# Performance work log

Measured on AMD Instinct MI355X. Metric: run time of the kernel, lower is better.

## Reference

```python
import jax, jax.numpy as jnp
from jax import lax
import numpy as np

B, T, H, W = 32, 16, 64, 64
LAT, HID, NL = 256, 256, 10
CH = 32  # c_hid
DN = ('NCHW', 'OIHW', 'NCHW')


def setup_inputs() -> dict:
    key = jax.random.key(0)
    keys = iter(jax.random.split(key, 64))
    def rn(shape, scale=0.05):
        return jax.random.normal(next(keys), shape, jnp.float32) * scale
    inp = {}
    inp['x'] = jax.random.normal(next(keys), (B, T, H, W), jnp.float32)
    inp['t'] = jax.random.normal(next(keys), (B, T, H, W), jnp.float32)
    # encoder convs (torch Conv2d weight layout: (out,in,kh,kw))
    inp['ec1_w'] = rn((CH, 1, 3, 3));        inp['ec1_b'] = rn((CH,))
    inp['ec2_w'] = rn((CH, CH, 3, 3));       inp['ec2_b'] = rn((CH,))
    inp['ec3_w'] = rn((2*CH, CH, 3, 3));     inp['ec3_b'] = rn((2*CH,))
    inp['ec4_w'] = rn((2*CH, 2*CH, 3, 3));   inp['ec4_b'] = rn((2*CH,))
    inp['ec5_w'] = rn((2*CH, 2*CH, 3, 3));   inp['ec5_b'] = rn((2*CH,))
    inp['el_w'] = rn((LAT, 2*CH*8*8));       inp['el_b'] = rn((LAT,))
    # decoder (ConvTranspose2d weight layout: (in,out,kh,kw))
    inp['dl_w'] = rn((2*CH*8*8, LAT));       inp['dl_b'] = rn((2*CH*8*8,))
    inp['dt1_w'] = rn((2*CH, 2*CH, 3, 3));   inp['dt1_b'] = rn((2*CH,))
    inp['dc1_w'] = rn((2*CH, 2*CH, 3, 3));   inp['dc1_b'] = rn((2*CH,))
    inp['dt2_w'] = rn((2*CH, CH, 3, 3));     inp['dt2_b'] = rn((CH,))
    inp['dc2_w'] = rn((CH, CH, 3, 3));       inp['dc2_b'] = rn((CH,))
    inp['dt3_w'] = rn((CH, 1, 3, 3));        inp['dt3_b'] = rn((1,))
    # 10 stacked LSTMCells (LAT == HID so layer 0 weight shape matches the rest)
    inp['Wih'] = rn((NL, 4*HID, HID))
    inp['Whh'] = rn((NL, 4*HID, HID))
    inp['bih'] = rn((NL, 4*HID))
    inp['bhh'] = rn((NL, 4*HID))
    inp['lw'] = rn((LAT, HID));  inp['lb'] = rn((LAT,))
    return inp


def gelu(v):
    return jax.nn.gelu(v, approximate=False)


def conv(x, w, b, stride):
    y = lax.conv_general_dilated(x, w, (stride, stride), [(1, 1), (1, 1)], dimension_numbers=DN)
    return y + b[None, :, None, None]


def tconv(x, w, b):
    # torch ConvTranspose2d(k=3, stride=2, padding=1, output_padding=1):
    # flip kernel, swap in/out channels, lhs_dilation=2, pad (lo=1, hi=2)
    wf = jnp.transpose(w[:, :, ::-1, ::-1], (1, 0, 2, 3))
    y = lax.conv_general_dilated(x, wf, (1, 1), [(1, 2), (1, 2)], lhs_dilation=(2, 2), dimension_numbers=DN)
    return y + b[None, :, None, None]


def reference(x, t, ec1_w, ec1_b, ec2_w, ec2_b, ec3_w, ec3_b, ec4_w, ec4_b, ec5_w, ec5_b,
              el_w, el_b, dl_w, dl_b, dt1_w, dt1_b, dc1_w, dc1_b, dt2_w, dt2_b,
              dc2_w, dc2_b, dt3_w, dt3_b, Wih, Whh, bih, bhh, lw, lb):

    def encode(imgs):                              # (N,1,64,64) -> (N,LAT)
        h = gelu(conv(imgs, ec1_w, ec1_b, 2))      # 32x32
        h = gelu(conv(h, ec2_w, ec2_b, 1))
        h = gelu(conv(h, ec3_w, ec3_b, 2))         # 16x16
        h = gelu(conv(h, ec4_w, ec4_b, 1))
        h = gelu(conv(h, ec5_w, ec5_b, 2))         # 8x8
        return h.reshape(h.shape[0], -1) @ el_w.T + el_b

    def decode(z):                                 # (N,LAT) -> (N,1,64,64)
        h = gelu(z @ dl_w.T + dl_b).reshape(z.shape[0], 2*CH, 8, 8)
        h = gelu(tconv(h, dt1_w, dt1_b))           # 16x16
        h = gelu(conv(h, dc1_w, dc1_b, 1))
        h = gelu(tconv(h, dt2_w, dt2_b))           # 32x32
        h = gelu(conv(h, dc2_w, dc2_b, 1))
        return jnp.tanh(tconv(h, dt3_w, dt3_b))    # 64x64

    def cell_stack(h, c, xin):                     # h,c: (NL,B,HID)
        hs, cs = [], []
        prev = xin
        for l in range(NL):
            z = prev @ Wih[l].T + bih[l] + h[l] @ Whh[l].T + bhh[l]
            i, f, g, o = jnp.split(z, 4, axis=-1)
            cl = jax.nn.sigmoid(f) * c[l] + jax.nn.sigmoid(i) * jnp.tanh(g)
            hl = jax.nn.sigmoid(o) * jnp.tanh(cl)
            hs.append(hl); cs.append(cl); prev = hl
        out = prev @ lw.T + lb                     # skip=False
        return jnp.stack(hs), jnp.stack(cs), out

    f_x_t = jnp.concatenate((x, t), axis=1)        # (B,2T,H,W)
    z_x_t = encode(f_x_t.reshape(-1, 1, H, W)).reshape(B, 2 * T, LAT)
    z_x = z_x_t[:, :T]

    h0 = jnp.zeros((NL, B, HID), x.dtype)
    c0 = jnp.zeros((NL, B, HID), x.dtype)

    def step1(carry, xin):
        h, c = carry
        h, c, out = cell_stack(h, c, xin)
        return (h, c), out

    (hT, cT), outs1 = lax.scan(step1, (h0, c0), jnp.swapaxes(z_x, 0, 1))

    def step2(carry, _):
        h, c, xin = carry
        h, c, out = cell_stack(h, c, xin)
        return (h, c, out), out

    _, outs2 = lax.scan(step2, (hT, cT, outs1[-1]), None, length=T)

    outputs = jnp.swapaxes(jnp.concatenate((outs1, outs2), axis=0), 0, 1)  # (B,2T,LAT)
    y_t = outputs[:, T - 1:-1]                    # (B,T,LAT)

    f_t_ = decode(y_t.reshape(B * T, LAT))        # (B*T,1,H,W)
    loss_pred = jnp.mean((f_t_ - f_x_t[:, T:].reshape(-1, 1, H, W)) ** 2)

    f_x_ = decode(z_x.reshape(B * T, LAT))        # rec_loss=True branch
    loss_rec = jnp.mean((f_x_ - f_x_t[:, :T].reshape(-1, 1, H, W)) ** 2)

    return loss_pred, loss_rec, f_t_.reshape(B, T, H, W)
```

## Files before the change

kernel.cpp:

```cpp
#include <hip/hip_runtime.h>
#include <math.h>

#define DEV __device__ __forceinline__

typedef __attribute__((ext_vector_type(8))) short bf8_t;
typedef __attribute__((ext_vector_type(4))) float f4_t;
typedef unsigned short us;

DEV float sigm_f(float v) { return 1.0f / (1.0f + __expf(-v)); }
DEV float tanh_f(float v) { return fmaf(-2.0f, 1.0f / (1.0f + __expf(2.0f * v)), 1.0f); }
DEV float gelu_f(float v) {
  float u = 0.79788456080f * fmaf(0.044715f * v * v, v, v);
  return 0.5f * v * (1.0f + tanh_f(u));
}
DEV unsigned short f2bf(float f) {
  unsigned u = __float_as_uint(f);
  u = (u + 0x7FFFu + ((u >> 16) & 1u)) >> 16;
  return (unsigned short)u;
}
DEV void astore(unsigned* p, unsigned v) {
  __hip_atomic_store(p, v, __ATOMIC_RELAXED, __HIP_MEMORY_SCOPE_AGENT);
}

DEV void prep_norm(int li, const float* w, us* wb, int CIN) {
// ... 19 lines not shown
    const float* __restrict__ ec2, const float* __restrict__ ec3,
    const float* __restrict__ ec4, const float* __restrict__ ec5,
    const float* __restrict__ dt1, const float* __restrict__ dc1,
    const float* __restrict__ dt2, const float* __restrict__ dc2,
    us* __restrict__ o_ec2, us* __restrict__ o_ec3,
    us* __restrict__ o_ec4, us* __restrict__ o_ec5,
    us* __restrict__ o_dt1, us* __restrict__ o_dc1,
    us* __restrict__ o_dt2, us* __restrict__ o_dc2)
{
  int idx = blockIdx.x * 256 + threadIdx.x;
  if (idx < 9216)        prep_norm(idx,          ec2, o_ec2, 32);
  else if (idx < 27648)  prep_norm(idx - 9216,   ec3, o_ec3, 32);
  else if (idx < 64512)  prep_norm(idx - 27648,  ec4, o_ec4, 64);
  else if (idx < 101376) prep_norm(idx - 64512,  ec5, o_ec5, 64);
  else if (idx < 138240) prep_par (idx - 101376, dt1, o_dt1, 64, 64);
  else if (idx < 175104) prep_norm(idx - 138240, dc1, o_dc1, 64);
  else if (idx < 193536) prep_par (idx - 175104, dt2, o_dt2, 32, 64);
  else if (idx < 202752) prep_norm(idx - 193536, dc2, o_dc2, 32);
}

__global__ __launch_bounds__(256) void prep_misc_k(
    const float* __restrict__ Wih, const float* __restrict__ lw,
    const float* __restrict__ lb,  const float* __restrict__ bih,
    us* __restrict__ wih0b, us* __restrict__ lwTb,
    us* __restrict__ lwbp,  float* __restrict__ beff)
{
  int idx = blockIdx.x * 256 + threadIdx.x;
  if (idx < 262144) {
    wih0b[idx] = f2bf(Wih[idx]);
  } else if (idx < 327680) {
    int i = idx - 262144;
    int n = i & 255, kcol = i >> 8;
    lwTb[i] = f2bf(lw[(size_t)n * 256 + kcol]);
  } else if (idx < 393216) {
    int i = idx - 327680;
    lwbp[i] = f2bf(lw[i]);
  } else if (idx < 394240) {
    int j = idx - 393216;
    float s = bih[j];
    const float* row = Wih + (size_t)j * 256;
    for (int n = 0; n < 256; ++n) s = fmaf(row[n], lb[n], s);
    beff[j] = s;
  }
}

__global__ __launch_bounds__(256) void prep_big_k(
    const float* __restrict__ el_w, const float* __restrict__ dl_w,
    const float* __restrict__ Wih,  const float* __restrict__ Whh,
    us* __restrict__ elWb, us* __restrict__ dlWb,
    us* __restrict__ wihb, us* __restrict__ whhb)
{
  int idx = blockIdx.x * 256 + threadIdx.x;
  if (idx < 1048576) {
    int i = idx;
    int kn = i & 4095, n = i >> 12;
    elWb[i] = f2bf(el_w[(size_t)n * 4096 + ((kn & 63) * 64 + (kn >> 6))]);
  } else if (idx < 2097152) {
    int i = idx - 1048576;
    int k = i & 255, nout = i >> 8;
    dlWb[i] = f2bf(dl_w[(size_t)((nout & 63) * 64 + (nout >> 6)) * 256 + k]);
  } else if (idx < 4718592) {
    int i = idx - 2097152;
    int e = i & 7, lane = (i >> 3) & 63, ks = (i >> 9) & 7;
    int nt = (i >> 12) & 63, l = i >> 18;
    wihb[i] = f2bf(Wih[((size_t)l * 1024 + nt * 16 + (lane & 15)) * 256
                       + ks * 32 + (lane >> 4) * 8 + e]);
  } else {
    int i = idx - 4718592;
    int e = i & 7, lane = (i >> 3) & 63, ks = (i >> 9) & 7;
    int nt = (i >> 12) & 63, l = i >> 18;
    whhb[i] = f2bf(Whh[((size_t)l * 1024 + nt * 16 + (lane & 15)) * 256
                       + ks * 32 + (lane >> 4) * 8 + e]);
  }
}

__global__ __launch_bounds__(256) void prep_wl1_k(
    const us* __restrict__ src, us* __restrict__ wb)
{
  int idx = blockIdx.x * 256 + threadIdx.x;
  int e = idx & 7, lane = (idx >> 3) & 63, ks = (idx >> 9) & 7, nt = idx >> 12;
  wb[idx] = src[(size_t)(nt * 16 + (lane & 15)) * 256 + ks * 32 + (lane >> 4) * 8 + e];
}

__global__ __launch_bounds__(256) void ec1_k(
    const float* __restrict__ x, const float* __restrict__ t,
    const float* __restrict__ w, const float* __restrict__ bias,
    us* __restrict__ out)
{
  __shared__ float sw[288];
  __shared__ float sb[32];
  for (int i = threadIdx.x; i < 288; i += 256) sw[i] = w[i];
  if (threadIdx.x < 32) sb[threadIdx.x] = bias[threadIdx.x];
  __syncthreads();
  int idx = blockIdx.x * 256 + threadIdx.x;
  int ox = idx & 31, oy = (idx >> 5) & 31, n = idx >> 10;
  int b = n >> 5, j = n & 31;
  const float* ip = (j < 16) ? (x + (size_t)(b * 16 + j) * 4096)
                             : (t + (size_t)(b * 16 + j - 16) * 4096);
  float pv[9];
#pragma unroll
  for (int kh = 0; kh < 3; ++kh) {
    int iy = oy * 2 + kh - 1;
#pragma unroll
    for (int kw = 0; kw < 3; ++kw) {
      int ix = ox * 2 + kw - 1;
      pv[kh * 3 + kw] = ((unsigned)iy < 64u && (unsigned)ix < 64u) ? ip[iy * 64 + ix] : 0.f;
    }
  }
  us u[32];
#pragma unroll
  for (int co = 0; co < 32; ++co) {
    float a = sb[co];
#pragma unroll
    for (int i = 0; i < 9; ++i) a = fmaf(pv[i], sw[co * 9 + i], a);
    u[co] = f2bf(gelu_f(a));
  }
  us* op = out + (size_t)idx * 32;
#pragma unroll
  for (int p = 0; p < 4; ++p) {
    uint4 v;
    v.x = u[p*8+0] | (u[p*8+1] << 16);
    v.y = u[p*8+2] | (u[p*8+3] << 16);
    v.z = u[p*8+4] | (u[p*8+5] << 16);
    v.w = u[p*8+6] | (u[p*8+7] << 16);
    *(uint4*)&op[p * 8] = v;
  }
}

template<int CIN, int COUT, int HIN, int WIN, int TH, int TW, int MODE>
DEV void convmf_tile(const us* __restrict__ in, const us* __restrict__ wb,
                     const float* __restrict__ bias, us* __restrict__ out,
                     int vb, int nofs, us* lds)
{
  constexpr int HO  = (MODE == 1) ? HIN / 2 : HIN;
  constexpr int WO  = (MODE == 1) ? WIN / 2 : WIN;
  constexpr int TIH = (MODE == 1) ? 2 * TH + 1 : TH + 2;
  constexpr int TIW = (MODE == 1) ? 2 * TW + 1 : TW + 2;
  constexpr int TIWP = (TIW & 1) ? TIW : TIW + 1;
  constexpr int CG  = CIN / 8;
  constexpr int K   = 9 * CIN;
  constexpr int KS  = K / 32;
  constexpr int NT  = COUT / 16;
  constexpr int MT  = (TH * TW) / 16;
  constexpr int MPW = MT / 4;
  constexpr int TY  = HO / TH, TX = WO / TW;

  const int n = nofs + vb / (TY * TX);
  const int trem = vb % (TY * TX);
  const int ty0 = (trem / TX) * TH, tx0 = (trem % TX) * TW;

  constexpr int ENT = TIH * TIW * CG;
  for (int e = threadIdx.x; e < ENT; e += 256) {
    int txx = e % TIW;
    int rr  = e / TIW;
    int cg  = rr % CG;
    int tyy = rr / CG;
    int iy, ix; bool ok;
    if (MODE == 0) {
      iy = ty0 + tyy - 1; ix = tx0 + txx - 1;
      ok = (unsigned)iy < (unsigned)HIN && (unsigned)ix < (unsigned)WIN;
    } else {
      iy = 2 * ty0 + tyy - 1; ix = 2 * tx0 + txx - 1;
      ok = (unsigned)iy < (unsigned)HIN && (unsigned)ix < (unsigned)WIN;
    }
    int4 val = {0, 0, 0, 0};
    if (ok) val = *(const int4*)&in[(((size_t)n * HIN + iy) * WIN + ix) * CIN + cg * 8];
    *(int4*)&lds[(size_t)((tyy * CG + cg) * TIWP + txx) * 8] = val;
  }
  __syncthreads();

  const int lane = threadIdx.x & 63, wv = threadIdx.x >> 6;
  const int l15 = lane & 15, l4 = lane >> 4;

  f4_t acc[MPW][NT] = {};
  for (int ks = 0; ks < KS; ++ks) {
    const int tap = (ks * 32) / CIN;
    const int kh = tap / 3, kw = tap % 3;
    const int cb = ((ks * 32) % CIN) / 8 + l4;
    bf8_t bf[NT];
#pragma unroll
    for (int nt = 0; nt < NT; ++nt)
      bf[nt] = *(const bf8_t*)&wb[(size_t)(nt * 16 + l15) * K + ks * 32 + 8 * l4];
#pragma unroll
    for (int mi = 0; mi < MPW; ++mi) {
      int m = (wv * MPW + mi) * 16 + l15;
      int oy = m / TW, ox = m % TW;
      int rt = ((MODE == 1) ? 2 * oy : oy) + kh;
      int ct = ((MODE == 1) ? 2 * ox : ox) + kw;
      bf8_t a = *(const bf8_t*)&lds[(size_t)((rt * CG + cb) * TIWP + ct) * 8];
#pragma unroll
      for (int nt = 0; nt < NT; ++nt)
        acc[mi][nt] = __builtin_amdgcn_mfma_f32_16x16x32_bf16(a, bf[nt], acc[mi][nt], 0, 0, 0);
    }
  }

#pragma unroll
  for (int mi = 0; mi < MPW; ++mi) {
    int mbase = (wv * MPW + mi) * 16;
#pragma unroll
    for (int nt = 0; nt < NT; ++nt) {
      int co = nt * 16 + l15;
      float bv = bias[co];
#pragma unroll
      for (int r = 0; r < 4; ++r) {
        int m = mbase + l4 * 4 + r;
        int oy = m / TW, ox = m % TW;
        float v = acc[mi][nt][r] + bv;
        out[(((size_t)n * HO + ty0 + oy) * WO + (tx0 + ox)) * COUT + co] = f2bf(gelu_f(v));
      }
    }
  }
  __syncthreads();
}

template<int CIN, int COUT, int HIN, int WIN, int TH, int TW, int MODE>
__global__ __launch_bounds__(256) void convmf_k(
    const us* __restrict__ in, const us* __restrict__ wb,
    const float* __restrict__ bias, us* __restrict__ out)
{
  constexpr int TIH = (MODE == 1) ? 2 * TH + 1 : TH + 2;
  constexpr int TIW = (MODE == 1) ? 2 * TW + 1 : TW + 2;
  constexpr int TIWP = (TIW & 1) ? TIW : TIW + 1;
  __shared__ us lds[TIH * TIWP * (CIN / 8) * 8];
  convmf_tile<CIN, COUT, HIN, WIN, TH, TW, MODE>(in, wb, bias, out, blockIdx.x, 0, lds);
}

template<int CIN, int COUT, int HIN, int WIN, int SH, int SW>
DEV void tconvp_tile(const us* __restrict__ in, const us* __restrict__ wbp,
                     const float* __restrict__ bias, us* __restrict__ out,
                     int vb, int nofs, us* lds)
{
  constexpr int HO = 2 * HIN, WO = 2 * WIN;
  constexpr int CG = CIN / 8;
  constexpr int TIH = SH + 1, TIW = SW + 1;
  constexpr int NT = COUT / 16;
  constexpr int MPW_P = (SH * SW) / 16;
  constexpr int TY = HIN / SH, TX = WIN / SW;

  const int n = nofs + vb / (TY * TX);
  const int trem = vb % (TY * TX);
  const int toy = trem / TX, tox = trem % TX;
  const int ty0s = toy * SH, tx0s = tox * SW;

  constexpr int ENT = TIH * TIW * CG;
  for (int e = threadIdx.x; e < ENT; e += 256) {
    int txx = e % TIW;
    int rr  = e / TIW;
    int cg  = rr % CG;
    int tyy = rr / CG;
    int iy = ty0s + tyy, ix = tx0s + txx;
    int4 val = {0, 0, 0, 0};
    if (iy < HIN && ix < WIN)
      val = *(const int4*)&in[(((size_t)n * HIN + iy) * WIN + ix) * CIN + cg * 8];
    *(int4*)&lds[(size_t)((tyy * CG + cg) * TIW + txx) * 8] = val;
  }
  __syncthreads();

  const int lane = threadIdx.x & 63, wv = threadIdx.x >> 6;
  const int l15 = lane & 15, l4 = lane >> 4;
  const int dy = wv >> 1, dx = wv & 1;
  const int NXT = 1 + dx;
  const int KS2 = ((1 + dy) * (1 + dx) * CIN) / 32;
  const int koff = (dy ? (dx ? 5 : 3) : (dx ? 1 : 0)) * CIN;

  f4_t acc[MPW_P][NT] = {};
  for (int ks = 0; ks < KS2; ++ks) {
    const int tapi = (ks * 32) / CIN;
    const int cb = ((ks * 32) % CIN) / 8 + l4;
    const int ra = tapi / NXT, rb = tapi % NXT;
    bf8_t bf[NT];
#pragma unroll
    for (int nt = 0; nt < NT; ++nt)
      bf[nt] = *(const bf8_t*)&wbp[(size_t)(nt * 16 + l15) * 9 * CIN + koff + ks * 32 + 8 * l4];
#pragma unroll
    for (int mi = 0; mi < MPW_P; ++mi) {
      int m = mi * 16 + l15;
      int i = m / SW, j = m % SW;
      bf8_t a = *(const bf8_t*)&lds[(size_t)(((i + ra) * CG + cb) * TIW + (j + rb)) * 8];
#pragma unroll
      for (int nt = 0; nt < NT; ++nt)
        acc[mi][nt] = __builtin_amdgcn_mfma_f32_16x16x32_bf16(a, bf[nt], acc[mi][nt], 0, 0, 0);
    }
  }

#pragma unroll
  for (int mi = 0; mi < MPW_P; ++mi) {
#pragma unroll
    for (int nt = 0; nt < NT; ++nt) {
      int co = nt * 16 + l15;
      float bv = bias[co];
#pragma unroll
      for (int r = 0; r < 4; ++r) {
        int m = mi * 16 + l4 * 4 + r;
        int i = m / SW, j = m % SW;
        int orow = 2 * (ty0s + i) + dy, ocol = 2 * (tx0s + j) + dx;
        float v = acc[mi][nt][r] + bv;
        out[(((size_t)n * HO + orow) * WO + ocol) * COUT + co] = f2bf(gelu_f(v));
      }
    }
  }
  __syncthreads();
}

template<int CIN, int COUT, int HIN, int WIN, int SH, int SW>
__global__ __launch_bounds__(256) void tconvp_k(
    const us* __restrict__ in, const us* __restrict__ wbp,
    const float* __restrict__ bias, us* __restrict__ out)
{
  __shared__ us lds[(SH + 1) * (SW + 1) * (CIN / 8) * 8];
  tconvp_tile<CIN, COUT, HIN, WIN, SH, SW>(in, wbp, bias, out, blockIdx.x, 0, lds);
}

template<int BIASMODE, bool GELU, int OUTMODE>
__global__ __launch_bounds__(256) void gemm16_k(
    const us* __restrict__ A, const us* __restrict__ Bw,
    const float* __restrict__ bias, void* __restrict__ Cv, int M, int N, int K)
{
  const int lane = threadIdx.x & 63, wv = threadIdx.x >> 6;
  const int l15 = lane & 15, l4 = lane >> 4;
  const int mbase = blockIdx.y * 64 + wv * 16;
  const int nbase = blockIdx.x * 64;
  f4_t acc[4] = {};
  for (int k0 = 0; k0 < K; k0 += 32) {
    bf8_t a = *(const bf8_t*)&A[(size_t)(mbase + l15) * K + k0 + 8 * l4];
#pragma unroll
    for (int nt = 0; nt < 4; ++nt) {
      bf8_t b = *(const bf8_t*)&Bw[(size_t)(nbase + nt * 16 + l15) * K + k0 + 8 * l4];
      acc[nt] = __builtin_amdgcn_mfma_f32_16x16x32_bf16(a, b, acc[nt], 0, 0, 0);
    }
  }
#pragma unroll
  for (int nt = 0; nt < 4; ++nt) {
    int col = nbase + nt * 16 + l15;
    float bv = 0.f;
    if (BIASMODE == 0) bv = bias[col];
    if (BIASMODE == 1) bv = bias[(col & 63) * 64 + (col >> 6)];
#pragma unroll
    for (int r = 0; r < 4; ++r) {
      int row = mbase + l4 * 4 + r;
      float v = acc[nt][r] + bv;
      if (GELU) v = gelu_f(v);
      if (OUTMODE == 0)      ((float*)Cv)[(size_t)row * N + col] = v;
      else if (OUTMODE == 1) ((us*)Cv)[(size_t)row * N + col] = f2bf(v);
      else {
        int orow = (row & 31) * 16 + (row >> 5);
        ((us*)Cv)[(size_t)orow * N + col] = f2bf(v);
      }
    }
  }
}

DEV void dlgemm_rec_tile(const us* __restrict__ A, const us* __restrict__ Bw,
                         const float* __restrict__ bias, us* __restrict__ C, int vb)
{
  const int lane = threadIdx.x & 63, wv = threadIdx.x >> 6;
  const int l15 = lane & 15, l4 = lane >> 4;
  const int mbase = 512 + (vb >> 6) * 64 + wv * 16;
  const int nbase = (vb & 63) * 64;
  f4_t acc[4] = {};
  for (int k0 = 0; k0 < 256; k0 += 32) {
    bf8_t a = *(const bf8_t*)&A[(size_t)(mbase + l15) * 256 + k0 + 8 * l4];
#pragma unroll
    for (int nt = 0; nt < 4; ++nt) {
      bf8_t b = *(const bf8_t*)&Bw[(size_t)(nbase + nt * 16 + l15) * 256 + k0 + 8 * l4];
      acc[nt] = __builtin_amdgcn_mfma_f32_16x16x32_bf16(a, b, acc[nt], 0, 0, 0);
    }
  }
#pragma unroll
  for (int nt = 0; nt < 4; ++nt) {
    int col = nbase + nt * 16 + l15;
    float bv = bias[(col & 63) * 64 + (col >> 6)];
#pragma unroll
    for (int r = 0; r < 4; ++r) {
      int row = mbase + l4 * 4 + r;
      C[(size_t)row * 4096 + col] = f2bf(gelu_f(acc[nt][r] + bv));
    }
  }
}

DEV void dt3_rec_tile(const us* __restrict__ in, const float* __restrict__ w,
                      const float* __restrict__ bias, const float* __restrict__ xref,
                      float* __restrict__ partials, int vb, float* sw, float* ws4)
{
  for (int i2 = threadIdx.x; i2 < 288; i2 += 256) sw[i2] = w[i2];
  __syncthreads();
  int idx = vb * 256 + threadIdx.x;
  int j = idx & 31, i = (idx >> 5) & 31, nl = idx >> 10;
  int n = 512 + nl;
  bool okj = (j < 31), oki = (i < 31);
  const us* r00 = in + (((size_t)n * 32 + i) * 32 + j) * 32;
  const us* r01 = r00 + 32;
  const us* r10 = r00 + 1024;
  const us* r11 = r10 + 32;
  float b0 = bias[0];
  float acc00 = b0, acc01 = b0, acc10 = b0, acc11 = b0;
  uint4 z4 = {0, 0, 0, 0};
#pragma unroll
  for (int g2 = 0; g2 < 4; ++g2) {
    uint4 v00 = *(const uint4*)&r00[g2 * 8];
    uint4 v01 = okj ? *(const uint4*)&r01[g2 * 8] : z4;
    uint4 v10 = oki ? *(const uint4*)&r10[g2 * 8] : z4;
    uint4 v11 = (oki && okj) ? *(const uint4*)&r11[g2 * 8] : z4;
    unsigned a00[4] = {v00.x, v00.y, v00.z, v00.w};
    unsigned a01[4] = {v01.x, v01.y, v01.z, v01.w};
    unsigned a10[4] = {v10.x, v10.y, v10.z, v10.w};
    unsigned a11[4] = {v11.x, v11.y, v11.z, v11.w};
#pragma unroll
    for (int h2 = 0; h2 < 4; ++h2) {
      int c0 = (g2 * 8 + h2 * 2) * 9;
      float xl, xh;
      xl = __uint_as_float(a00[h2] << 16); xh = __uint_as_float(a00[h2] & 0xffff0000u);
      acc00 = fmaf(xl, sw[c0 + 4], acc00); acc00 = fmaf(xh, sw[c0 + 13], acc00);
      acc01 = fmaf(xl, sw[c0 + 5], acc01); acc01 = fmaf(xh, sw[c0 + 14], acc01);
      acc10 = fmaf(xl, sw[c0 + 7], acc10); acc10 = fmaf(xh, sw[c0 + 16], acc10);
      acc11 = fmaf(xl, sw[c0 + 8], acc11); acc11 = fmaf(xh, sw[c0 + 17], acc11);
      xl = __uint_as_float(a01[h2] << 16); xh = __uint_as_float(a01[h2] & 0xffff0000u);
      acc01 = fmaf(xl, sw[c0 + 3], acc01); acc01 = fmaf(xh, sw[c0 + 12], acc01);
      acc11 = fmaf(xl, sw[c0 + 6], acc11); acc11 = fmaf(xh, sw[c0 + 15], acc11);
      xl = __uint_as_float(a10[h2] << 16); xh = __uint_as_float(a10[h2] & 0xffff0000u);
      acc10 = fmaf(xl, sw[c0 + 1], acc10); acc10 = fmaf(xh, sw[c0 + 10], acc10);
      acc11 = fmaf(xl, sw[c0 + 2], acc11); acc11 = fmaf(xh, sw[c0 + 11], acc11);
      xl = __uint_as_float(a11[h2] << 16); xh = __uint_as_float(a11[h2] & 0xffff0000u);
      acc11 = fmaf(xl, sw[c0 + 0], acc11); acc11 = fmaf(xh, sw[c0 + 9], acc11);
    }
  }
  float o00 = tanh_f(acc00), o01 = tanh_f(acc01);
  float o10 = tanh_f(acc10), o11 = tanh_f(acc11);
  size_t px = (size_t)(2 * i) * 64 + 2 * j;
  const float* xr = xref + (size_t)nl * 4096;
  float d0 = o00 - xr[px],      d1 = o01 - xr[px + 1];
  float d2 = o10 - xr[px + 64], d3 = o11 - xr[px + 65];
  float s = d0 * d0 + d1 * d1 + d2 * d2 + d3 * d3;
#pragma unroll
  for (int off = 32; off > 0; off >>= 1) s += __shfl_down(s, off);
  if ((threadIdx.x & 63) == 0) ws4[threadIdx.x >> 6] = s;
  __syncthreads();
  if (threadIdx.x == 0) partials[2048 + vb] = ws4[0] + ws4[1] + ws4[2] + ws4[3];
  __syncthreads();
}

__global__ __launch_bounds__(256) void dt3_loss_k(
    const us* __restrict__ in, const float* __restrict__ w,
    const float* __restrict__ bias, const float* __restrict__ tref,
    float* __restrict__ fout, float* __restrict__ partials)
{
  __shared__ float sw[288];
  for (int i2 = threadIdx.x; i2 < 288; i2 += 256) sw[i2] = w[i2];
  __syncthreads();
  int idx = blockIdx.x * 256 + threadIdx.x;
  int j = idx & 31, i = (idx >> 5) & 31, n = idx >> 10;
  bool okj = (j < 31), oki = (i < 31);
  const us* r00 = in + (((size_t)n * 32 + i) * 32 + j) * 32;
  const us* r01 = r00 + 32;
  const us* r10 = r00 + 1024;
  const us* r11 = r10 + 32;
  float b0 = bias[0];
  float acc00 = b0, acc01 = b0, acc10 = b0, acc11 = b0;
  uint4 z4 = {0, 0, 0, 0};
#pragma unroll
  for (int g2 = 0; g2 < 4; ++g2) {
    uint4 v00 = *(const uint4*)&r00[g2 * 8];
    uint4 v01 = okj ? *(const uint4*)&r01[g2 * 8] : z4;
    uint4 v10 = oki ? *(const uint4*)&r10[g2 * 8] : z4;
    uint4 v11 = (oki && okj) ? *(const uint4*)&r11[g2 * 8] : z4;
    unsigned a00[4] = {v00.x, v00.y, v00.z, v00.w};
    unsigned a01[4] = {v01.x, v01.y, v01.z, v01.w};
    unsigned a10[4] = {v10.x, v10.y, v10.z, v10.w};
    unsigned a11[4] = {v11.x, v11.y, v11.z, v11.w};
#pragma unroll
    for (int h2 = 0; h2 < 4; ++h2) {
      int c0 = (g2 * 8 + h2 * 2) * 9;
      float xl, xh;
      xl = __uint_as_float(a00[h2] << 16); xh = __uint_as_float(a00[h2] & 0xffff0000u);
      acc00 = fmaf(xl, sw[c0 + 4], acc00); acc00 = fmaf(xh, sw[c0 + 13], acc00);
      acc01 = fmaf(xl, sw[c0 + 5], acc01); acc01 = fmaf(xh, sw[c0 + 14], acc01);
      acc10 = fmaf(xl, sw[c0 + 7], acc10); acc10 = fmaf(xh, sw[c0 + 16], acc10);
      acc11 = fmaf(xl, sw[c0 + 8], acc11); acc11 = fmaf(xh, sw[c0 + 17], acc11);
      xl = __uint_as_float(a01[h2] << 16); xh = __uint_as_float(a01[h2] & 0xffff0000u);
      acc01 = fmaf(xl, sw[c0 + 3], acc01); acc01 = fmaf(xh, sw[c0 + 12], acc01);
      acc11 = fmaf(xl, sw[c0 + 6], acc11); acc11 = fmaf(xh, sw[c0 + 15], acc11);
      xl = __uint_as_float(a10[h2] << 16); xh = __uint_as_float(a10[h2] & 0xffff0000u);
      acc10 = fmaf(xl, sw[c0 + 1], acc10); acc10 = fmaf(xh, sw[c0 + 10], acc10);
      acc11 = fmaf(xl, sw[c0 + 2], acc11); acc11 = fmaf(xh, sw[c0 + 11], acc11);
      xl = __uint_as_float(a11[h2] << 16); xh = __uint_as_float(a11[h2] & 0xffff0000u);
      acc11 = fmaf(xl, sw[c0 + 0], acc11); acc11 = fmaf(xh, sw[c0 + 9], acc11);
    }
  }
  float o00 = tanh_f(acc00), o01 = tanh_f(acc01);
  float o10 = tanh_f(acc10), o11 = tanh_f(acc11);
  size_t px = (size_t)(2 * i) * 64 + 2 * j;
  float* fb = fout + (size_t)n * 4096;
  fb[px] = o00;      fb[px + 1] = o01;
  fb[px + 64] = o10; fb[px + 65] = o11;
  const float* tr = tref + (size_t)n * 4096;
  float d0 = o00 - tr[px],      d1 = o01 - tr[px + 1];
  float d2 = o10 - tr[px + 64], d3 = o11 - tr[px + 65];
  float s = d0 * d0 + d1 * d1 + d2 * d2 + d3 * d3;
#pragma unroll
  for (int off = 32; off > 0; off >>= 1) s += __shfl_down(s, off);
  __shared__ float ws4[4];
  if ((threadIdx.x & 63) == 0) ws4[threadIdx.x >> 6] = s;
  __syncthreads();
  if (threadIdx.x == 0) partials[blockIdx.x] = ws4[0] + ws4[1] + ws4[2] + ws4[3];
}

__global__ __launch_bounds__(256) void loss_final_k(
    const float* __restrict__ partials, float* __restrict__ out01)
{
  __shared__ float red[256];
  int base = blockIdx.x * 2048;
  float s = 0.f;
  for (int i = threadIdx.x; i < 2048; i += 256) s += partials[base + i];
  red[threadIdx.x] = s;
  __syncthreads();
#pragma unroll
  for (int st = 128; st > 0; st >>= 1) {
    if (threadIdx.x < st) red[threadIdx.x] += red[threadIdx.x + st];
    __syncthreads();
  }
  if (threadIdx.x == 0) out01[blockIdx.x] = red[0] * (1.0f / 2097152.0f);
}

__global__ __launch_bounds__(256) void gather_z_k(
    const float* __restrict__ z, us* __restrict__ ydec)
{
  int idx = blockIdx.x * 256 + threadIdx.x;
  int rr = idx >> 8, k = idx & 255;
  int b = rr >> 4, tt = rr & 15;
  ydec[(size_t)(512 + rr) * 256 + k] = f2bf(z[(size_t)(b * 32 + tt) * 256 + k]);
}

#define LSTM_NB 160

DEV void gridbar(unsigned* bar, unsigned target) {
  __syncthreads();
  if (threadIdx.x == 0) {
    __hip_atomic_fetch_add(bar, 1u, __ATOMIC_RELEASE, __HIP_MEMORY_SCOPE_AGENT);
    unsigned spins = 0;
    while (__hip_atomic_load(bar, __ATOMIC_RELAXED, __HIP_MEMORY_SCOPE_AGENT) < target) {
      __builtin_amdgcn_s_sleep(2);
      if (++spins > (1u << 24)) break;
    }
    (void)__hip_atomic_load(bar, __ATOMIC_ACQUIRE, __HIP_MEMORY_SCOPE_AGENT);
  }
  __syncthreads();
}

DEV void spin_min16s(unsigned* f, unsigned tgt) {
  if ((int)tgt <= 0) return;
  unsigned spins = 0;
  for (;;) {
    unsigned m = 0xffffffffu;
#pragma unroll
    for (int i = 0; i < 16; ++i) {
      unsigned v = __hip_atomic_load(f + i * 32, __ATOMIC_RELAXED, __HIP_MEMORY_SCOPE_AGENT);
      m = v < m ? v : m;
    }
    if (m >= tgt) return;
    if (++spins > (1u << 22)) return;
  }
}

__global__ __launch_bounds__(256, 1) void mega_k(
    const float* __restrict__ z, const us* __restrict__ wihb,
    const us* __restrict__ whhb, const us* __restrict__ meffb,
    const float* __restrict__ bih, const float* __restrict__ bhh,
    const float* __restrict__ beff,
    us* __restrict__ zbf, us* __restrict__ hbf, us* __restrict__ h9sav,
    unsigned* __restrict__ bar,
    const us* __restrict__ ydec, const us* __restrict__ dlWb,
    const float* __restrict__ dl_b,
    const us* __restrict__ wbp_dt1, const float* __restrict__ dt1_b,
    const us* __restrict__ wb_dc1,  const float* __restrict__ dc1_b,
    const us* __restrict__ wbp_dt2, const float* __restrict__ dt2_b,
    const us* __restrict__ wb_dc2,  const float* __restrict__ dc2_b,
    const float* __restrict__ dt3_w, const float* __restrict__ dt3_b,
    const float* __restrict__ xref,
    us* __restrict__ bufA, us* __restrict__ bufB,
    float* __restrict__ partials)
{
  __shared__ __align__(16) unsigned char smem[109568];

  const int tid = threadIdx.x;
  const int bid = blockIdx.x;

  if (bid < 160) {
    us*    s_w   = (us*)smem;
    us*    s_x   = (us*)(smem + 65536);
    us*    s_h   = (us*)(smem + 81920);
    float* zsm   = (float*)(smem + 98304);
    float* cls   = (float*)(smem + 107008);
    float* sbias = (float*)(smem + 109056);
    float* sb2   = (float*)(smem + 109312);

    const int l   = bid >> 4;
    const int jg  = bid & 15;
    const int col0 = jg * 16;
    const int lane = tid & 63, g = tid >> 6;
    const int l15 = lane & 15, l4 = lane >> 4;
    const int gtid = bid * 256 + tid;

    unsigned* fl = bar + 64;
    unsigned* fown = fl + (size_t)l * 16 * 32;

    for (int i = gtid; i < 16 * 32 * 256; i += LSTM_NB * 256) {
      int k = i & 255, r = i >> 8;
      int tt = r >> 5, b = r & 31;
      zbf[i] = f2bf(z[(size_t)(b * 32 + tt) * 256 + k]);
    }
    for (int i = gtid; i < 81920; i += LSTM_NB * 256) hbf[81920 + i] = 0;
    for (int c = tid; c < 4096; c += 256) {
      int gm = c >> 9;
      int gg = gm >> 1, m = gm & 1;
      int c2 = c & 511;
      const us* src = (m == 0 ? wihb : whhb)
          + ((size_t)(l * 64 + gg * 16 + jg) * 8) * 512;
      *(int4*)&s_w[(size_t)c * 8] = *(const int4*)&src[(size_t)c2 * 8];
    }
    for (int i = tid; i < 512; i += 256) cls[i] = 0.f;
    if (tid < 64) {
      int gg = tid >> 4, j = tid & 15;
      sbias[tid] = bih[l * 1024 + gg * 256 + col0 + j]
                 + bhh[l * 1024 + gg * 256 + col0 + j];
      sb2[tid]   = beff[gg * 256 + col0 + j] + bhh[gg * 256 + col0 + j];
    }

    gridbar(bar, LSTM_NB);

    for (int t = 0; t <= 30; ++t) {
      const int cur = t & 1, prv = cur ^ 1;
      const bool p2 = (t >= 16);
      const bool p2l0 = p2 && (l == 0);

      if (tid == 0) {
        spin_min16s(fown, (unsigned)t);
        (void)__hip_atomic_load(fown, __ATOMIC_ACQUIRE, __HIP_MEMORY_SCOPE_AGENT);
      }
      __syncthreads();
      const us* hb = hbf + (size_t)((prv * 10 + l) * 32) * 256;
#pragma unroll
      for (int i = 0; i < 4; ++i) {
        int c = tid + i * 256;
        int sw = (c & ~31) | ((c & 31) ^ ((c >> 5) & 7));
        *(int4*)&s_h[(size_t)sw * 8] = *(const int4*)&hb[(size_t)c * 8];
      }
      if (tid == 0) {
        if (l == 0) {
          if (t >= 16) spin_min16s(fl + (size_t)9 * 16 * 32, (unsigned)t);
        } else {
          spin_min16s(fl + (size_t)(l - 1) * 16 * 32, (unsigned)(t + 1));
        }
        if (t >= 2) {
          if (l < 9) spin_min16s(fl + (size_t)(l + 1) * 16 * 32, (unsigned)(t - 1));
          else if (t >= 17) spin_min16s(fl, (unsigned)t);
        }
        (void)__hip_atomic_load(fown, __ATOMIC_ACQUIRE, __HIP_MEMORY_SCOPE_AGENT);
      }
      __syncthreads();
      const us* xb =
          (l == 0) ? (p2 ? (hbf + (size_t)((prv * 10 + 9) * 32) * 256)
                         : (zbf + (size_t)t * 32 * 256))
                   : (hbf + (size_t)((cur * 10 + l - 1) * 32) * 256);
#pragma unroll
      for (int i = 0; i < 4; ++i) {
        int c = tid + i * 256;
        int sw = (c & ~31) | ((c & 31) ^ ((c >> 5) & 7));
        *(int4*)&s_x[(size_t)sw * 8] = *(const int4*)&xb[(size_t)c * 8];
      }
      __syncthreads();
      f4_t a0 = {}, a1 = {}, b0 = {}, b1 = {};
#pragma unroll
      for (int ks = 0; ks < 8; ++ks) {
        bf8_t bwi = *(const bf8_t*)&s_w[(size_t)((g * 2 + 0) * 4096 + ks * 512 + lane * 8)];
        bf8_t bwh = *(const bf8_t*)&s_w[(size_t)((g * 2 + 1) * 4096 + ks * 512 + lane * 8)];
        int cx0 = (l15 << 5) | ((ks * 4 + l4) ^ (l15 & 7));
        int cx1 = ((16 + l15) << 5) | ((ks * 4 + l4) ^ (l15 & 7));
        bf8_t ax0 = *(const bf8_t*)&s_x[(size_t)cx0 * 8];
        bf8_t ax1 = *(const bf8_t*)&s_x[(size_t)cx1 * 8];
        bf8_t ah0 = *(const bf8_t*)&s_h[(size_t)cx0 * 8];
        bf8_t ah1 = *(const bf8_t*)&s_h[(size_t)cx1 * 8];
        a0 = __builtin_amdgcn_mfma_f32_16x16x32_bf16(ax0, bwi, a0, 0, 0, 0);
        a1 = __builtin_amdgcn_mfma_f32_16x16x32_bf16(ax1, bwi, a1, 0, 0, 0);
        b0 = __builtin_amdgcn_mfma_f32_16x16x32_bf16(ah0, bwh, b0, 0, 0, 0);
        b1 = __builtin_amdgcn_mfma_f32_16x16x32_bf16(ah1, bwh, b1, 0, 0, 0);
      }
#pragma unroll
      for (int r = 0; r < 4; ++r) {
        zsm[(g * 32 + l4 * 4 + r) * 17 + l15] = a0[r] + b0[r];
        zsm[(g * 32 + 16 + l4 * 4 + r) * 17 + l15] = a1[r] + b1[r];
      }
      __syncthreads();
#pragma unroll
      for (int half = 0; half < 2; ++half) {
        int e = tid + half * 256;
        int b = e >> 4, j = e & 15;
        float zi = zsm[(0 * 32 + b) * 17 + j] + (p2l0 ? sb2[j]      : sbias[j]);
        float zf = zsm[(1 * 32 + b) * 17 + j] + (p2l0 ? sb2[16 + j] : sbias[16 + j]);
        float zg = zsm[(2 * 32 + b) * 17 + j] + (p2l0 ? sb2[32 + j] : sbias[32 + j]);
        float zo = zsm[(3 * 32 + b) * 17 + j] + (p2l0 ? sb2[48 + j] : sbias[48 + j]);
        float cold = cls[b * 16 + j];
        float cn = sigm_f(zf) * cold + sigm_f(zi) * tanh_f(zg);
        cls[b * 16 + j] = cn;
        float hn = sigm_f(zo) * tanh_f(cn);
        float hn_hi = __shfl_down(hn, 1);
        if (!(j & 1)) {
          unsigned pk = (unsigned)f2bf(hn) | ((unsigned)f2bf(hn_hi) << 16);
          astore((unsigned*)&hbf[(size_t)((cur * 10 + l) * 32 + b) * 256 + col0 + j], pk);
          if (l == 9 && t >= 15)
            astore((unsigned*)&h9sav[(size_t)((t - 15) * 32 + b) * 256 + col0 + j], pk);
        }
      }
      __syncthreads();
      if (tid == 0)
        __hip_atomic_store(&fown[jg * 32], (unsigned)(t + 1),
                           __ATOMIC_RELEASE, __HIP_MEMORY_SCOPE_AGENT);
      if (l == 0 && t == 15) {
        for (int c = tid; c < 2048; c += 256) {
          int gg = c >> 9, c2 = c & 511;
          const us* src = meffb + ((size_t)(gg * 16 + jg) * 8) * 512;
          *(int4*)&s_w[(size_t)((gg * 2) * 512 + c2) * 8] = *(const int4*)&src[(size_t)c2 * 8];
        }
        __syncthreads();
      }
    }
  } else {
    us* lds = (us*)smem;
    float* swq = (float*)(smem + 49152);
    float* ws4 = (float*)(smem + 50432);
    unsigned* bar96 = bar + 32;
    const int wg = bid - 160;
    int ep2 = 0;

    for (int vb = wg; vb < 512; vb += 96)
      dlgemm_rec_tile(ydec, dlWb, dl_b, bufB, vb);
    ++ep2; gridbar(bar96, (unsigned)(ep2 * 96));
    for (int vb = wg; vb < 512; vb += 96)
      tconvp_tile<64, 64, 8, 8, 8, 8>(bufB, wbp_dt1, dt1_b, bufA, vb, 512, lds);
    ++ep2; gridbar(bar96, (unsigned)(ep2 * 96));
    for (int vb = wg; vb < 512; vb += 96)
      convmf_tile<64, 64, 16, 16, 16, 16, 0>(bufA, wb_dc1, dc1_b, bufB, vb, 512, lds);
    ++ep2; gridbar(bar96, (unsigned)(ep2 * 96));
    for (int vb = wg; vb < 1024; vb += 96)
      tconvp_tile<64, 32, 16, 16, 8, 16>(bufB, wbp_dt2, dt2_b, bufA, vb, 512, lds);
    ++ep2; gridbar(bar96, (unsigned)(ep2 * 96));
    for (int vb = wg; vb < 2048; vb += 96)
      convmf_tile<32, 32, 32, 32, 16, 16, 0>(bufA, wb_dc2, dc2_b, bufB, vb, 512, lds);
    ++ep2; gridbar(bar96, (unsigned)(ep2 * 96));
    for (int vb = wg; vb < 2048; vb += 96)
      dt3_rec_tile(bufB, dt3_w, dt3_b, xref, partials, vb, swq, ws4);
  }
}

extern "C" void kernel_launch(void* const* d_in, const int* in_sizes, int n_in,
                              void* d_out, int out_size, void* d_ws, size_t ws_size,
                              hipStream_t stream) {
  const float* x     = (const float*)d_in[0];
  const float* t     = (const float*)d_in[1];
  const float* ec1_w = (const float*)d_in[2];
  const float* ec1_b = (const float*)d_in[3];
  const float* ec2_w = (const float*)d_in[4];
  const float* ec2_b = (const float*)d_in[5];
  const float* ec3_w = (const float*)d_in[6];
  const float* ec3_b = (const float*)d_in[7];
  const float* ec4_w = (const float*)d_in[8];
  const float* ec4_b = (const float*)d_in[9];
  const float* ec5_w = (const float*)d_in[10];
  const float* ec5_b = (const float*)d_in[11];
  const float* el_w  = (const float*)d_in[12];
  const float* el_b  = (const float*)d_in[13];
  const float* dl_w  = (const float*)d_in[14];
  const float* dl_b  = (const float*)d_in[15];
  const float* dt1_w = (const float*)d_in[16];
  const float* dt1_b = (const float*)d_in[17];
  const float* dc1_w = (const float*)d_in[18];
  const float* dc1_b = (const float*)d_in[19];
  const float* dt2_w = (const float*)d_in[20];
  const float* dt2_b = (const float*)d_in[21];
  const float* dc2_w = (const float*)d_in[22];
  const float* dc2_b = (const float*)d_in[23];
  const float* dt3_w = (const float*)d_in[24];
  const float* dt3_b = (const float*)d_in[25];
  const float* Wih   = (const float*)d_in[26];
  const float* Whh   = (const float*)d_in[27];
  const float* bih   = (const float*)d_in[28];
  const float* bhh   = (const float*)d_in[29];
  const float* lw    = (const float*)d_in[30];
  const float* lb    = (const float*)d_in[31];
  float* out = (float*)d_out;

  char* base = (char*)d_ws;
  size_t off = 0;
  auto alloc = [&](size_t bytes) -> char* {
    char* p = base + off;
    off += (bytes + 255) & ~(size_t)255;
    return p;
  };
  unsigned* bar   = (unsigned*)alloc(32768);
  float* zbuf     = (float*)alloc((size_t)1024 * 256 * 4);
  us*    zbf      = (us*)alloc((size_t)16 * 32 * 256 * 2);
  us*    hbf      = (us*)alloc((size_t)2 * 10 * 32 * 256 * 2);
  us*    h9sav    = (us*)alloc((size_t)16 * 32 * 256 * 2);
  us*    ydec     = (us*)alloc((size_t)1024 * 256 * 2);
  float* partials = (float*)alloc((size_t)16384 * 4);
  us* wb_ec2 = (us*)alloc((size_t)32 * 288 * 2);
  us* wb_ec3 = (us*)alloc((size_t)64 * 288 * 2);
  us* wb_ec4 = (us*)alloc((size_t)64 * 576 * 2);
  us* wb_ec5 = (us*)alloc((size_t)64 * 576 * 2);
  us* wbp_dt1 = (us*)alloc((size_t)64 * 576 * 2);
  us* wb_dc1 = (us*)alloc((size_t)64 * 576 * 2);
  us* wbp_dt2 = (us*)alloc((size_t)32 * 576 * 2);
  us* wb_dc2 = (us*)alloc((size_t)32 * 288 * 2);
  us* elWb   = (us*)alloc((size_t)256 * 4096 * 2);
  us* dlWb   = (us*)alloc((size_t)4096 * 256 * 2);
  us* wihb   = (us*)alloc((size_t)10 * 1024 * 256 * 2);
  us* whhb   = (us*)alloc((size_t)10 * 1024 * 256 * 2);
  us* wih0b  = (us*)alloc((size_t)1024 * 256 * 2);
  us* lwTb   = (us*)alloc((size_t)256 * 256 * 2);
  us* lwbp   = (us*)alloc((size_t)256 * 256 * 2);
  us* meffp  = (us*)alloc((size_t)1024 * 256 * 2);
  us* meffb  = (us*)alloc((size_t)1024 * 256 * 2);
  float* beff = (float*)alloc((size_t)1024 * 4);
  us* enc5   = (us*)alloc((size_t)1024 * 4096 * 2);
  us* bufA   = (us*)alloc((size_t)1024 * 32 * 32 * 32 * 2);
  us* bufB   = (us*)alloc((size_t)1024 * 32 * 32 * 32 * 2);
  (void)in_sizes; (void)n_in; (void)out_size; (void)ws_size;

  hipMemsetAsync(bar, 0, 32768, stream);

  prepw_all_k<<<792, 256, 0, stream>>>(ec2_w, ec3_w, ec4_w, ec5_w,
                                       dt1_w, dc1_w, dt2_w, dc2_w,
                                       wb_ec2, wb_ec3, wb_ec4, wb_ec5,
                                       wbp_dt1, wb_dc1, wbp_dt2, wb_dc2);
  prep_misc_k<<<1540, 256, 0, stream>>>(Wih, lw, lb, bih, wih0b, lwTb, lwbp, beff);
  prep_big_k<<<28672, 256, 0, stream>>>(el_w, dl_w, Wih, Whh, elWb, dlWb, wihb, whhb);
  gemm16_k<2, false, 1><<<dim3(4, 16), 256, 0, stream>>>(wih0b, lwTb, lb, meffp, 1024, 256, 256);
  prep_wl1_k<<<1024, 256, 0, stream>>>(meffp, meffb);

  ec1_k<<<4096, 256, 0, stream>>>(x, t, ec1_w, ec1_b, bufA);
  convmf_k<32, 32, 32, 32, 16, 16, 0><<<4096, 256, 0, stream>>>(bufA, wb_ec2, ec2_b, bufB);
  convmf_k<32, 64, 32, 32, 16, 16, 1><<<1024, 256, 0, stream>>>(bufB, wb_ec3, ec3_b, bufA);
  convmf_k<64, 64, 16, 16, 16, 16, 0><<<1024, 256, 0, stream>>>(bufA, wb_ec4, ec4_b, bufB);
  convmf_k<64, 64, 16, 16, 8, 8, 1><<<1024, 256, 0, stream>>>(bufB, wb_ec5, ec5_b, enc5);
  gemm16_k<0, false, 0><<<dim3(4, 16), 256, 0, stream>>>(enc5, elWb, el_b, zbuf, 1024, 256, 4096);

  gather_z_k<<<512, 256, 0, stream>>>(zbuf, ydec);

  mega_k<<<256, 256, 0, stream>>>(zbuf, wihb, whhb, meffb, bih, bhh, beff,
                                  zbf, hbf, h9sav, bar,
                                  ydec, dlWb, dl_b,
                                  wbp_dt1, dt1_b, wb_dc1, dc1_b,
                                  wbp_dt2, dt2_b, wb_dc2, dc2_b,
                                  dt3_w, dt3_b, x, bufA, bufB, partials);

  gemm16_k<0, false, 2><<<dim3(4, 8), 256, 0, stream>>>(
      h9sav, lwbp, lb, ydec, 512, 256, 256);
  gemm16_k<1, true, 1><<<dim3(64, 8), 256, 0, stream>>>(ydec, dlWb, dl_b, bufB, 1024, 4096, 256);
  tconvp_k<64, 64, 8, 8, 8, 8><<<512, 256, 0, stream>>>(bufB, wbp_dt1, dt1_b, bufA);
  convmf_k<64, 64, 16, 16, 16, 16, 0><<<512, 256, 0, stream>>>(bufA, wb_dc1, dc1_b, bufB);
  tconvp_k<64, 32, 16, 16, 8, 16><<<1024, 256, 0, stream>>>(bufB, wbp_dt2, dt2_b, bufA);
  convmf_k<32, 32, 32, 32, 16, 16, 0><<<2048, 256, 0, stream>>>(bufA, wb_dc2, dc2_b, bufB);
  dt3_loss_k<<<2048, 256, 0, stream>>>(bufB, dt3_w, dt3_b, t, out + 2, partials);
  loss_final_k<<<2, 256, 0, stream>>>(partials, out);
}
```

Before: 1.264 ms.

## Fold prediction decoder and loss reduction into persistent mega kernel

The separate trailing launches are removed: the output-projection GEMM, dl GEMM, transposed convs, convs, final dt3+loss stage and loss reduction. They now run as extra phases inside the persistent mega kernel, separated by grid barriers across all 256 workgroups. This cuts the launch overhead and the gaps between kernels. In exchange each phase runs on only 256 workgroups with large LDS per block, which may give lower parallelism than the original 2048-block grids, plus a grid-barrier cost per phase.

```diff
diff --git a/kernel.cpp b/kernel.cpp
--- a/kernel.cpp
+++ b/kernel.cpp
@@ -345,15 +345,6 @@
   __syncthreads();
 }
 
-template<int CIN, int COUT, int HIN, int WIN, int SH, int SW>
-__global__ __launch_bounds__(256) void tconvp_k(
-    const us* __restrict__ in, const us* __restrict__ wbp,
-    const float* __restrict__ bias, us* __restrict__ out)
-{
-  __shared__ us lds[(SH + 1) * (SW + 1) * (CIN / 8) * 8];
-  tconvp_tile<CIN, COUT, HIN, WIN, SH, SW>(in, wbp, bias, out, blockIdx.x, 0, lds);
-}
-
 template<int BIASMODE, bool GELU, int OUTMODE>
 __global__ __launch_bounds__(256) void gemm16_k(
     const us* __restrict__ A, const us* __restrict__ Bw,
@@ -393,12 +384,42 @@
   }
 }
 
-DEV void dlgemm_rec_tile(const us* __restrict__ A, const us* __restrict__ Bw,
-                         const float* __restrict__ bias, us* __restrict__ C, int vb)
+DEV void outsgemm_tile(const us* __restrict__ A, const us* __restrict__ Bw,
+                       const float* __restrict__ bias, us* __restrict__ ydec, int vb)
 {
   const int lane = threadIdx.x & 63, wv = threadIdx.x >> 6;
   const int l15 = lane & 15, l4 = lane >> 4;
-  const int mbase = 512 + (vb >> 6) * 64 + wv * 16;
+  const int mbase = (vb >> 2) * 64 + wv * 16;
+  const int nbase = (vb & 3) * 64;
+  f4_t acc[4] = {};
+  for (int k0 = 0; k0 < 256; k0 += 32) {
+    bf8_t a = *(const bf8_t*)&A[(size_t)(mbase + l15) * 256 + k0 + 8 * l4];
+#pragma unroll
+    for (int nt = 0; nt < 4; ++nt) {
+      bf8_t b = *(const bf8_t*)&Bw[(size_t)(nbase + nt * 16 + l15) * 256 + k0 + 8 * l4];
+      acc[nt] = __builtin_amdgcn_mfma_f32_16x16x32_bf16(a, b, acc[nt], 0, 0, 0);
+    }
+  }
+#pragma unroll
+  for (int nt = 0; nt < 4; ++nt) {
+    int col = nbase + nt * 16 + l15;
+    float bv = bias[col];
+#pragma unroll
+    for (int r = 0; r < 4; ++r) {
+      int row = mbase + l4 * 4 + r;
+      int orow = (row & 31) * 16 + (row >> 5);
+      ydec[(size_t)orow * 256 + col] = f2bf(acc[nt][r] + bv);
+    }
+  }
+}
+
+DEV void dlgemm_tile(const us* __restrict__ A, const us* __restrict__ Bw,
+                     const float* __restrict__ bias, us* __restrict__ C,
+                     int vb, int rofs)
+{
+  const int lane = threadIdx.x & 63, wv = threadIdx.x >> 6;
+  const int l15 = lane & 15, l4 = lane >> 4;
+  const int mbase = rofs + (vb >> 6) * 64 + wv * 16;
   const int nbase = (vb & 63) * 64;
   f4_t acc[4] = {};
   for (int k0 = 0; k0 < 256; k0 += 32) {
@@ -421,15 +442,17 @@
   }
 }
 
-DEV void dt3_rec_tile(const us* __restrict__ in, const float* __restrict__ w,
-                      const float* __restrict__ bias, const float* __restrict__ xref,
-                      float* __restrict__ partials, int vb, float* sw, float* ws4)
+template<int PRED>
+DEV void dt3_tile(const us* __restrict__ in, const float* __restrict__ w,
+                  const float* __restrict__ bias, const float* __restrict__ ref,
+                  float* __restrict__ fout, float* __restrict__ partials,
+                  int vb, float* sw, float* ws4)
 {
   for (int i2 = threadIdx.x; i2 < 288; i2 += 256) sw[i2] = w[i2];
   __syncthreads();
   int idx = vb * 256 + threadIdx.x;
   int j = idx & 31, i = (idx >> 5) & 31, nl = idx >> 10;
-  int n = 512 + nl;
+  int n = PRED ? nl : (512 + nl);
   bool okj = (j < 31), oki = (i < 31);
   const us* r00 = in + (((size_t)n * 32 + i) * 32 + j) * 32;
   const us* r01 = r00 + 32;
@@ -470,98 +493,21 @@
   float o00 = tanh_f(acc00), o01 = tanh_f(acc01);
   float o10 = tanh_f(acc10), o11 = tanh_f(acc11);
   size_t px = (size_t)(2 * i) * 64 + 2 * j;
-  const float* xr = xref + (size_t)nl * 4096;
-  float d0 = o00 - xr[px],      d1 = o01 - xr[px + 1];
-  float d2 = o10 - xr[px + 64], d3 = o11 - xr[px + 65];
+  if (PRED) {
+    float* fb = fout + (size_t)nl * 4096;
+    fb[px] = o00;      fb[px + 1] = o01;
+    fb[px + 64] = o10; fb[px + 65] = o11;
+  }
+  const float* rr = ref + (size_t)nl * 4096;
+  float d0 = o00 - rr[px],      d1 = o01 - rr[px + 1];
+  float d2 = o10 - rr[px + 64], d3 = o11 - rr[px + 65];
   float s = d0 * d0 + d1 * d1 + d2 * d2 + d3 * d3;
 #pragma unroll
   for (int off = 32; off > 0; off >>= 1) s += __shfl_down(s, off);
   if ((threadIdx.x & 63) == 0) ws4[threadIdx.x >> 6] = s;
   __syncthreads();
-  if (threadIdx.x == 0) partials[2048 + vb] = ws4[0] + ws4[1] + ws4[2] + ws4[3];
-  __syncthreads();
-}
-
-__global__ __launch_bounds__(256) void dt3_loss_k(
-    const us* __restrict__ in, const float* __restrict__ w,
-    const float* __restrict__ bias, const float* __restrict__ tref,
-    float* __restrict__ fout, float* __restrict__ partials)
-{
-  __shared__ float sw[288];
-  for (int i2 = threadIdx.x; i2 < 288; i2 += 256) sw[i2] = w[i2];
-  __syncthreads();
-  int idx = blockIdx.x * 256 + threadIdx.x;
-  int j = idx & 31, i = (idx >> 5) & 31, n = idx >> 10;
-  bool okj = (j < 31), oki = (i < 31);
-  const us* r00 = in + (((size_t)n * 32 + i) * 32 + j) * 32;
-  const us* r01 = r00 + 32;
-  const us* r10 = r00 + 1024;
-  const us* r11 = r10 + 32;
-  float b0 = bias[0];
-  float acc00 = b0, acc01 = b0, acc10 = b0, acc11 = b0;
-  uint4 z4 = {0, 0, 0, 0};
-#pragma unroll
-  for (int g2 = 0; g2 < 4; ++g2) {
-    uint4 v00 = *(const uint4*)&r00[g2 * 8];
-    uint4 v01 = okj ? *(const uint4*)&r01[g2 * 8] : z4;
-    uint4 v10 = oki ? *(const uint4*)&r10[g2 * 8] : z4;
-    uint4 v11 = (oki && okj) ? *(const uint4*)&r11[g2 * 8] : z4;
-    unsigned a00[4] = {v00.x, v00.y, v00.z, v00.w};
-    unsigned a01[4] = {v01.x, v01.y, v01.z, v01.w};
-    unsigned a10[4] = {v10.x, v10.y, v10.z, v10.w};
-    unsigned a11[4] = {v11.x, v11.y, v11.z, v11.w};
-#pragma unroll
-    for (int h2 = 0; h2 < 4; ++h2) {
-      int c0 = (g2 * 8 + h2 * 2) * 9;
-      float xl, xh;
-      xl = __uint_as_float(a00[h2] << 16); xh = __uint_as_float(a00[h2] & 0xffff0000u);
-      acc00 = fmaf(xl, sw[c0 + 4], acc00); acc00 = fmaf(xh, sw[c0 + 13], acc00);
-      acc01 = fmaf(xl, sw[c0 + 5], acc01); acc01 = fmaf(xh, sw[c0 + 14], acc01);
-      acc10 = fmaf(xl, sw[c0 + 7], acc10); acc10 = fmaf(xh, sw[c0 + 16], acc10);
-      acc11 = fmaf(xl, sw[c0 + 8], acc11); acc11 = fmaf(xh, sw[c0 + 17], acc11);
-      xl = __uint_as_float(a01[h2] << 16); xh = __uint_as_float(a01[h2] & 0xffff0000u);
-      acc01 = fmaf(xl, sw[c0 + 3], acc01); acc01 = fmaf(xh, sw[c0 + 12], acc01);
-      acc11 = fmaf(xl, sw[c0 + 6], acc11); acc11 = fmaf(xh, sw[c0 + 15], acc11);
-      xl = __uint_as_float(a10[h2] << 16); xh = __uint_as_float(a10[h2] & 0xffff0000u);
-      acc10 = fmaf(xl, sw[c0 + 1], acc10); acc10 = fmaf(xh, sw[c0 + 10], acc10);
-      acc11 = fmaf(xl, sw[c0 + 2], acc11); acc11 = fmaf(xh, sw[c0 + 11], acc11);
-      xl = __uint_as_float(a11[h2] << 16); xh = __uint_as_float(a11[h2] & 0xffff0000u);
-      acc11 = fmaf(xl, sw[c0 + 0], acc11); acc11 = fmaf(xh, sw[c0 + 9], acc11);
-    }
-  }
-  float o00 = tanh_f(acc00), o01 = tanh_f(acc01);
-  float o10 = tanh_f(acc10), o11 = tanh_f(acc11);
-  size_t px = (size_t)(2 * i) * 64 + 2 * j;
-  float* fb = fout + (size_t)n * 4096;
-  fb[px] = o00;      fb[px + 1] = o01;
-  fb[px + 64] = o10; fb[px + 65] = o11;
-  const float* tr = tref + (size_t)n * 4096;
-  float d0 = o00 - tr[px],      d1 = o01 - tr[px + 1];
-  float d2 = o10 - tr[px + 64], d3 = o11 - tr[px + 65];
-  float s = d0 * d0 + d1 * d1 + d2 * d2 + d3 * d3;
-#pragma unroll
-  for (int off = 32; off > 0; off >>= 1) s += __shfl_down(s, off);
-  __shared__ float ws4[4];
-  if ((threadIdx.x & 63) == 0) ws4[threadIdx.x >> 6] = s;
-  __syncthreads();
-  if (threadIdx.x == 0) partials[blockIdx.x] = ws4[0] + ws4[1] + ws4[2] + ws4[3];
-}
-
-__global__ __launch_bounds__(256) void loss_final_k(
-    const float* __restrict__ partials, float* __restrict__ out01)
-{
-  __shared__ float red[256];
-  int base = blockIdx.x * 2048;
-  float s = 0.f;
-  for (int i = threadIdx.x; i < 2048; i += 256) s += partials[base + i];
-  red[threadIdx.x] = s;
-  __syncthreads();
-#pragma unroll
-  for (int st = 128; st > 0; st >>= 1) {
-    if (threadIdx.x < st) red[threadIdx.x] += red[threadIdx.x + st];
-    __syncthreads();
-  }
-  if (threadIdx.x == 0) out01[blockIdx.x] = red[0] * (1.0f / 2097152.0f);
+  if (threadIdx.x == 0) partials[(PRED ? 0 : 2048) + vb] = ws4[0] + ws4[1] + ws4[2] + ws4[3];
+  __syncthreads();
 }
 
 __global__ __launch_bounds__(256) void gather_z_k(
@@ -611,16 +557,18 @@
     const float* __restrict__ beff,
     us* __restrict__ zbf, us* __restrict__ hbf, us* __restrict__ h9sav,
     unsigned* __restrict__ bar,
-    const us* __restrict__ ydec, const us* __restrict__ dlWb,
+    us* __restrict__ ydec, const us* __restrict__ dlWb,
     const float* __restrict__ dl_b,
+    const us* __restrict__ lwbp, const float* __restrict__ lb,
     const us* __restrict__ wbp_dt1, const float* __restrict__ dt1_b,
     const us* __restrict__ wb_dc1,  const float* __restrict__ dc1_b,
     const us* __restrict__ wbp_dt2, const float* __restrict__ dt2_b,
     const us* __restrict__ wb_dc2,  const float* __restrict__ dc2_b,
     const float* __restrict__ dt3_w, const float* __restrict__ dt3_b,
-    const float* __restrict__ xref,
+    const float* __restrict__ xref, const float* __restrict__ tref,
     us* __restrict__ bufA, us* __restrict__ bufB,
-    float* __restrict__ partials)
+    float* __restrict__ fout, float* __restrict__ partials,
+    float* __restrict__ out01)
 {
   __shared__ __align__(16) unsigned char smem[109568];
 
@@ -775,7 +723,7 @@
     int ep2 = 0;
 
     for (int vb = wg; vb < 512; vb += 96)
-      dlgemm_rec_tile(ydec, dlWb, dl_b, bufB, vb);
+      dlgemm_tile(ydec, dlWb, dl_b, bufB, vb, 512);
     ++ep2; gridbar(bar96, (unsigned)(ep2 * 96));
     for (int vb = wg; vb < 512; vb += 96)
       tconvp_tile<64, 64, 8, 8, 8, 8>(bufB, wbp_dt1, dt1_b, bufA, vb, 512, lds);
@@ -790,7 +738,52 @@
       convmf_tile<32, 32, 32, 32, 16, 16, 0>(bufA, wb_dc2, dc2_b, bufB, vb, 512, lds);
     ++ep2; gridbar(bar96, (unsigned)(ep2 * 96));
     for (int vb = wg; vb < 2048; vb += 96)
-      dt3_rec_tile(bufB, dt3_w, dt3_b, xref, partials, vb, swq, ws4);
+      dt3_tile<0>(bufB, dt3_w, dt3_b, xref, fout, partials, vb, swq, ws4);
+  }
+
+  {
+    us* lds = (us*)smem;
+    float* swq = (float*)(smem + 49152);
+    float* ws4 = (float*)(smem + 50432);
+    unsigned* barP = bar + 6144;
+    unsigned epP = 0;
+
+    ++epP; gridbar(barP, 256u * epP);
+    for (int vb = bid; vb < 32; vb += 256)
+      outsgemm_tile(h9sav, lwbp, lb, ydec, vb);
+    ++epP; gridbar(barP, 256u * epP);
+    for (int vb = bid; vb < 512; vb += 256)
+      dlgemm_tile(ydec, dlWb, dl_b, bufB, vb, 0);
+    ++epP; gridbar(barP, 256u * epP);
+    for (int vb = bid; vb < 512; vb += 256)
+      tconvp_tile<64, 64, 8, 8, 8, 8>(bufB, wbp_dt1, dt1_b, bufA, vb, 0, lds);
+    ++epP; gridbar(barP, 256u * epP);
+    for (int vb = bid; vb < 512; vb += 256)
+      convmf_tile<64, 64, 16, 16, 16, 16, 0>(bufA, wb_dc1, dc1_b, bufB, vb, 0, lds);
+    ++epP; gridbar(barP, 256u * epP);
+    for (int vb = bid; vb < 1024; vb += 256)
+      tconvp_tile<64, 32, 16, 16, 8, 16>(bufB, wbp_dt2, dt2_b, bufA, vb, 0, lds);
+    ++epP; gridbar(barP, 256u * epP);
+    for (int vb = bid; vb < 2048; vb += 256)
+      convmf_tile<32, 32, 32, 32, 16, 16, 0>(bufA, wb_dc2, dc2_b, bufB, vb, 0, lds);
+    ++epP; gridbar(barP, 256u * epP);
+    for (int vb = bid; vb < 2048; vb += 256)
+      dt3_tile<1>(bufB, dt3_w, dt3_b, tref, fout, partials, vb, swq, ws4);
+    ++epP; gridbar(barP, 256u * epP);
+    if (bid < 2) {
+      float* red = (float*)smem;
+      int base = bid * 2048;
+      float s = 0.f;
+      for (int i = tid; i < 2048; i += 256) s += partials[base + i];
+      red[tid] = s;
+      __syncthreads();
+#pragma unroll
+      for (int st = 128; st > 0; st >>= 1) {
+        if (tid < st) red[tid] += red[tid + st];
+        __syncthreads();
+      }
+      if (tid == 0) out01[bid] = red[0] * (1.0f / 2097152.0f);
+    }
   }
 }
 
@@ -890,18 +883,9 @@
 
   mega_k<<<256, 256, 0, stream>>>(zbuf, wihb, whhb, meffb, bih, bhh, beff,
                                   zbf, hbf, h9sav, bar,
-                                  ydec, dlWb, dl_b,
+                                  ydec, dlWb, dl_b, lwbp, lb,
                                   wbp_dt1, dt1_b, wb_dc1, dc1_b,
                                   wbp_dt2, dt2_b, wb_dc2, dc2_b,
-                                  dt3_w, dt3_b, x, bufA, bufB, partials);
-
-  gemm16_k<0, false, 2><<<dim3(4, 8), 256, 0, stream>>>(
-      h9sav, lwbp, lb, ydec, 512, 256, 256);
-  gemm16_k<1, true, 1><<<dim3(64, 8), 256, 0, stream>>>(ydec, dlWb, dl_b, bufB, 1024, 4096, 256);
-  tconvp_k<64, 64, 8, 8, 8, 8><<<512, 256, 0, stream>>>(bufB, wbp_dt1, dt1_b, bufA);
-  convmf_k<64, 64, 16, 16, 16, 16, 0><<<512, 256, 0, stream>>>(bufA, wb_dc1, dc1_b, bufB);
-  tconvp_k<64, 32, 16, 16, 8, 16><<<1024, 256, 0, stream>>>(bufB, wbp_dt2, dt2_b, bufA);
-  convmf_k<32, 32, 32, 32, 16, 16, 0><<<2048, 256, 0, stream>>>(bufA, wb_dc2, dc2_b, bufB);
-  dt3_loss_k<<<2048, 256, 0, stream>>>(bufB, dt3_w, dt3_b, t, out + 2, partials);
-  loss_final_k<<<2, 256, 0, stream>>>(partials, out);
-}
+                                  dt3_w, dt3_b, x, t,
+                                  bufA, bufB, out + 2, partials, out);
+}
```

After: 1.742 ms. +37.8%, slower.
